# Optimization experiments

Hardware: AMD Instinct MI355X
Metric: run time of the kernel (lower is better)

Reference implementation:

```python
import jax, jax.numpy as jnp
import numpy as np

NUM_FEATURES = 1024
NUM_TRAINING = 32768
NUM_EPOCHS = 2
STEP_SIZE = 0.01


def setup_inputs() -> dict:
    key = jax.random.key(0)
    k1, k2, k3 = jax.random.split(key, 3)
    data = jax.random.normal(k1, (NUM_TRAINING, NUM_FEATURES), dtype=jnp.float32)
    label = jax.random.uniform(k2, (NUM_TRAINING,), dtype=jnp.float32)
    theta = jax.random.normal(k3, (NUM_FEATURES,), dtype=jnp.float32)
    return {"data": data, "label": label, "theta": theta}


def reference(data, label, theta):
    data_2d = data.reshape(NUM_TRAINING, NUM_FEATURES)

    def sample_step(theta, xs):
        x, y = xs  # x: [F], y: scalar
        prob = jax.nn.sigmoid(jnp.dot(theta, x))
        theta = theta - STEP_SIZE * (prob - y) * x
        return theta, None

    def epoch_step(theta, _):
        theta, _ = jax.lax.scan(sample_step, theta, (data_2d, label))
        return theta, None

    theta, _ = jax.lax.scan(epoch_step, theta, None, length=NUM_EPOCHS)
    return theta
```

## Files before the change

### kernel.cpp

```cpp
#include <hip/hip_runtime.h>
#include <hip/hip_cooperative_groups.h>

namespace cg = cooperative_groups;

#define F 1024
#define NTRAIN 32768
#define EPOCHS 2
#define STEP 0.01f
#define BB 512
#define NBLK (NTRAIN / BB)
#define PHASES (EPOCHS * NBLK)
#define COOP_WGS 32

#define NL2E 1.4426950408889634f
#define C1K  0.014426950408889634f
#define NLN2 0.69314718055994531f

__device__ __forceinline__ float rdlane(float v, int lane) {
    return __uint_as_float(__builtin_amdgcn_readlane(__float_as_uint(v), (unsigned)lane));
}

__global__ __launch_bounds__(256) void gram_kernel(const float* __restrict__ X,
                                                   float* __restrict__ G,
                                                   float* __restrict__ C,
                                                   int tiles_per_b)
{
    const int wg  = blockIdx.x;
    const int b   = wg / tiles_per_b;
    int rem = wg % tiles_per_b;

    int ti, tj;
    bool isC = (rem >= 36);
    if (!isC) {
        int tij = rem; ti = 0;
        while (tij >= 8 - ti) { tij -= 8 - ti; ++ti; }
        tj = ti + tij;
    } else {
        rem -= 36; ti = rem >> 3; tj = rem & 7;
    }

    __shared__ __align__(16) float At[16][68];
    __shared__ __align__(16) float Bt[16][68];

    const int t  = threadIdx.x;
    const int tx = t & 15, ty = t >> 4;
    const int sr = t >> 2, sc = (t & 3) * 4;

    const int rowBlk = isC ? ((b + 1) & (NBLK - 1)) : b;
    const float* Xa = X + (size_t)(rowBlk * BB + ti * 64) * F;
    const float* Xb = X + (size_t)(b * BB + tj * 64) * F;
    float* Ob = (isC ? C : G) + (size_t)b * BB * BB;

    float acc[4][4];
#pragma unroll
    for (int p = 0; p < 4; ++p)
#pragma unroll
        for (int q = 0; q < 4; ++q) acc[p][q] = 0.f;

    for (int kc = 0; kc < F; kc += 16) {
        float4 va = *(const float4*)(Xa + (size_t)sr * F + kc + sc);
        float4 vb = *(const float4*)(Xb + (size_t)sr * F + kc + sc);
        __syncthreads();
        At[sc + 0][sr] = va.x; At[sc + 1][sr] = va.y; At[sc + 2][sr] = va.z; At[sc + 3][sr] = va.w;
        Bt[sc + 0][sr] = vb.x; Bt[sc + 1][sr] = vb.y; Bt[sc + 2][sr] = vb.z; Bt[sc + 3][sr] = vb.w;
        __syncthreads();
#pragma unroll
        for (int k = 0; k < 16; ++k) {
            float4 a4 = *(const float4*)&At[k][ty * 4];
            float4 b4 = *(const float4*)&Bt[k][tx * 4];
            acc[0][0] = fmaf(a4.x, b4.x, acc[0][0]);
            acc[0][1] = fmaf(a4.x, b4.y, acc[0][1]);
            acc[0][2] = fmaf(a4.x, b4.z, acc[0][2]);
            acc[0][3] = fmaf(a4.x, b4.w, acc[0][3]);
            acc[1][0] = fmaf(a4.y, b4.x, acc[1][0]);
            acc[1][1] = fmaf(a4.y, b4.y, acc[1][1]);
            acc[1][2] = fmaf(a4.y, b4.z, acc[1][2]);
            acc[1][3] = fmaf(a4.y, b4.w, acc[1][3]);
            acc[2][0] = fmaf(a4.z, b4.x, acc[2][0]);
            acc[2][1] = fmaf(a4.z, b4.y, acc[2][1]);
            acc[2][2] = fmaf(a4.z, b4.z, acc[2][2]);
            acc[2][3] = fmaf(a4.z, b4.w, acc[2][3]);
            acc[3][0] = fmaf(a4.w, b4.x, acc[3][0]);
            acc[3][1] = fmaf(a4.w, b4.y, acc[3][1]);
            acc[3][2] = fmaf(a4.w, b4.z, acc[3][2]);
            acc[3][3] = fmaf(a4.w, b4.w, acc[3][3]);
        }
    }

#pragma unroll
    for (int p = 0; p < 4; ++p) {
        int i = ti * 64 + ty * 4 + p;
        float4 v = make_float4(acc[p][0], acc[p][1], acc[p][2], acc[p][3]);
        *(float4*)(Ob + (size_t)i * BB + tj * 64 + tx * 4) = v;
    }
    if (!isC && ti != tj) {
#pragma unroll
        for (int p = 0; p < 4; ++p)
#pragma unroll
            for (int q = 0; q < 4; ++q)
                Ob[(size_t)(tj * 64 + tx * 4 + q) * BB + ti * 64 + ty * 4 + p] = acc[p][q];
    }
}

__global__ __launch_bounds__(256) void sgd_coop2(
    const float* __restrict__ X, const float* __restrict__ label,
    const float* __restrict__ theta0, float* __restrict__ out,
    const float* __restrict__ G, const float* __restrict__ C,
    float* __restrict__ theta, float* __restrict__ sbuf,
    float* __restrict__ spre, float* __restrict__ wbuf)
{
    cg::grid_group grid = cg::this_grid();
    const int tid = threadIdx.x;
    const int wg  = blockIdx.x;

    if (wg < 4) theta[wg * 256 + tid] = theta0[wg * 256 + tid];
    grid.sync();

    {
        const int wv = (wg << 2) | (tid >> 6);
        const int L  = tid & 63;
        const float4* th4 = (const float4*)theta;
        float4 t4[4];
#pragma unroll
        for (int m = 0; m < 4; ++m) t4[m] = th4[L + 64 * m];
        for (int rr = 0; rr < 4; ++rr) {
            const int r = wv * 4 + rr;
            const float4* xr = (const float4*)(X + (size_t)r * F);
            float acc = 0.f;
#pragma unroll
            for (int m = 0; m < 4; ++m) {
                float4 x4 = xr[L + 64 * m];
                acc = fmaf(x4.x, t4[m].x, acc);
                acc = fmaf(x4.y, t4[m].y, acc);
                acc = fmaf(x4.z, t4[m].z, acc);
                acc = fmaf(x4.w, t4[m].w, acc);
            }
#pragma unroll
            for (int off = 32; off > 0; off >>= 1)
                acc += __shfl_xor(acc, off, 64);
            if (L == 0) sbuf[r] = acc;
        }
    }
    grid.sync();

    for (int p = 0; p < PHASES; ++p) {
        const int blk = p & (NBLK - 1);

        if (wg == 0) {
            if (tid < 64) {
                const int L = tid;
                const float* Gb = G + (size_t)blk * BB * BB;
                const float4* s4 = (const float4*)sbuf;
                float4 z04 = s4[L * 2], z14 = s4[L * 2 + 1];
                float zac[8] = {-NL2E * z04.x, -NL2E * z04.y, -NL2E * z04.z, -NL2E * z04.w,
                                -NL2E * z14.x, -NL2E * z14.y, -NL2E * z14.z, -NL2E * z14.w};
                const float4* y4 = (const float4*)(label + blk * BB);
                float4 ya = y4[L * 2], yb = y4[L * 2 + 1];
                float c2[8] = {-C1K * ya.x, -C1K * ya.y, -C1K * ya.z, -C1K * ya.w,
                               -C1K * yb.x, -C1K * yb.y, -C1K * yb.z, -C1K * yb.w};

                float4 gb0[8], gb1[8];
#pragma unroll
                for (int u = 0; u < 8; ++u) {
                    const float4* gr = (const float4*)(Gb + (size_t)u * BB) + L * 2;
                    gb0[u] = gr[0]; gb1[u] = gr[1];
                }

                for (int i8 = 0; i8 < 64; ++i8) {
                    float wout[8];
#pragma unroll
                    for (int u = 0; u < 8; ++u) {
                        float zs = rdlane(zac[u], i8);
                        float cc = rdlane(c2[u], i8);
                        float E    = __builtin_amdgcn_exp2f(zs);
                        float prob = __builtin_amdgcn_rcpf(1.0f + E);
                        float wv2  = fmaf(C1K, prob, cc);
                        wout[u] = wv2 * -NLN2;
                        float ga[8] = {gb0[u].x, gb0[u].y, gb0[u].z, gb0[u].w,
                                       gb1[u].x, gb1[u].y, gb1[u].z, gb1[u].w};
#pragma unroll
                        for (int jj = 0; jj < 8; ++jj) {
                            int j = (u + 1 + jj) & 7;
                            zac[j] = fmaf(wv2, ga[j], zac[j]);
                        }
                        if (i8 < 63) {
                            const float4* gr =
                                (const float4*)(Gb + (size_t)((i8 + 1) * 8 + u) * BB) + L * 2;
                            gb0[u] = gr[0]; gb1[u] = gr[1];
                        }
                    }
                    if (L == i8) {
                        float4* wp = (float4*)(wbuf + i8 * 8);
                        wp[0] = make_float4(wout[0], wout[1], wout[2], wout[3]);
                        wp[1] = make_float4(wout[4], wout[5], wout[6], wout[7]);
                    }
                }
            }
        } else if (p + 1 < PHASES) {
            const int w = (wg - 1) * 4 + (tid >> 6);
            const int L = tid & 63;
            const int nblk = (p + 1) & (NBLK - 1);
            const float4* th4 = (const float4*)theta;
            float4 t4[4];
#pragma unroll
            for (int m = 0; m < 4; ++m) t4[m] = th4[L + 64 * m];
            for (int r = w; r < BB; r += 124) {
                const float4* xr = (const float4*)(X + (size_t)(nblk * BB + r) * F);
                float acc = 0.f;
#pragma unroll
                for (int m = 0; m < 4; ++m) {
                    float4 x4 = xr[L + 64 * m];
                    acc = fmaf(x4.x, t4[m].x, acc);
                    acc = fmaf(x4.y, t4[m].y, acc);
                    acc = fmaf(x4.z, t4[m].z, acc);
                    acc = fmaf(x4.w, t4[m].w, acc);
                }
#pragma unroll
                for (int off = 32; off > 0; off >>= 1)
                    acc += __shfl_xor(acc, off, 64);
                if (L == 0) spre[r] = acc;
            }
        }
        grid.sync();

        if (wg < 16) {
            __shared__ float red[4][64];
            const int j  = wg * 64 + (tid & 63);
            const int rg = tid >> 6;
            const float* Xb = X + (size_t)blk * BB * F;
            float acc = 0.f;
            for (int ii = 0; ii < 128; ++ii) {
                const int i = rg * 128 + ii;
                acc = fmaf(wbuf[i], Xb[(size_t)i * F + j], acc);
            }
            red[rg][tid & 63] = acc;
            __syncthreads();
            if (tid < 64) {
                float v = theta[j] + red[0][tid] + red[1][tid] + red[2][tid] + red[3][tid];
                theta[j] = v;
                if (p == PHASES - 1) out[j] = v;
            }
        } else if (p + 1 < PHASES) {
            const int w2 = (wg - 16) * 4 + (tid >> 6);
            const int L  = tid & 63;
            const float* Cb = C + (size_t)blk * BB * BB;
            const float4* w4 = (const float4*)wbuf;
            float4 wa = w4[L * 2], wb4 = w4[L * 2 + 1];
            for (int rr = 0; rr < 8; ++rr) {
                const int r = w2 * 8 + rr;
                const float4* cr = (const float4*)(Cb + (size_t)r * BB) + L * 2;
                float4 c0 = cr[0], c1r = cr[1];
                float acc = c0.x * wa.x;
                acc = fmaf(c0.y, wa.y, acc);
                acc = fmaf(c0.z, wa.z, acc);
                acc = fmaf(c0.w, wa.w, acc);
                acc = fmaf(c1r.x, wb4.x, acc);
                acc = fmaf(c1r.y, wb4.y, acc);
                acc = fmaf(c1r.z, wb4.z, acc);
                acc = fmaf(c1r.w, wb4.w, acc);
#pragma unroll
                for (int off = 32; off > 0; off >>= 1)
                    acc += __shfl_xor(acc, off, 64);
                if (L == 0) sbuf[r] = spre[r] + acc;
            }
        }
        grid.sync();
    }
}

__global__ __launch_bounds__(256) void sgd_coop(
    const float* __restrict__ X, const float* __restrict__ label,
    const float* __restrict__ theta0, float* __restrict__ out,
    const float* __restrict__ G, float* __restrict__ theta,
    float* __restrict__ sbuf, float* __restrict__ wbuf)
{
    cg::grid_group grid = cg::this_grid();
    const int tid = threadIdx.x;
    const int wg  = blockIdx.x;

    if (wg < 4) theta[wg * 256 + tid] = theta0[wg * 256 + tid];
    grid.sync();

    auto sgemv = [&](int blk) {
        const int wv = (wg << 2) | (tid >> 6);
        const int L  = tid & 63;
        const float4* th4 = (const float4*)theta;
        float4 t4[4];
#pragma unroll
        for (int m = 0; m < 4; ++m) t4[m] = th4[L + 64 * m];
        for (int rr = 0; rr < 4; ++rr) {
            const int r = wv * 4 + rr;
            const float4* xr = (const float4*)(X + (size_t)(blk * BB + r) * F);
            float acc = 0.f;
#pragma unroll
            for (int m = 0; m < 4; ++m) {
                float4 x4 = xr[L + 64 * m];
                acc = fmaf(x4.x, t4[m].x, acc);
                acc = fmaf(x4.y, t4[m].y, acc);
                acc = fmaf(x4.z, t4[m].z, acc);
                acc = fmaf(x4.w, t4[m].w, acc);
            }
#pragma unroll
            for (int off = 32; off > 0; off >>= 1)
                acc += __shfl_xor(acc, off, 64);
            if (L == 0) sbuf[r] = acc;
        }
    };

    sgemv(0);
    grid.sync();

    for (int p = 0; p < PHASES; ++p) {
        const int blk = p & (NBLK - 1);
        if (wg == 0 && tid < 64) {
            const int L = tid;
            const float* Gb = G + (size_t)blk * BB * BB;
            const float4* s4 = (const float4*)sbuf;
            float4 z04 = s4[L * 2], z14 = s4[L * 2 + 1];
            float zac[8] = {z04.x, z04.y, z04.z, z04.w, z14.x, z14.y, z14.z, z14.w};
            const float4* y4 = (const float4*)(label + blk * BB);
            float4 ya = y4[L * 2], yb = y4[L * 2 + 1];
            float yv[8] = {ya.x, ya.y, ya.z, ya.w, yb.x, yb.y, yb.z, yb.w};
            float4 gb0[8], gb1[8];
#pragma unroll
            for (int u = 0; u < 8; ++u) {
                const float4* gr = (const float4*)(Gb + (size_t)u * BB) + L * 2;
                gb0[u] = gr[0]; gb1[u] = gr[1];
            }
            for (int i8 = 0; i8 < 64; ++i8) {
                float wout[8];
#pragma unroll
                for (int u = 0; u < 8; ++u) {
                    float zi = rdlane(zac[u], i8);
                    float yi = rdlane(yv[u], i8);
                    float E    = __builtin_amdgcn_exp2f(zi * -NL2E);
                    float prob = __builtin_amdgcn_rcpf(1.0f + E);
                    float wv   = STEP * (yi - prob);
                    wout[u] = wv;
                    float4 g0 = gb0[u], g1 = gb1[u];
                    zac[0] = fmaf(wv, g0.x, zac[0]);
                    zac[1] = fmaf(wv, g0.y, zac[1]);
                    zac[2] = fmaf(wv, g0.z, zac[2]);
                    zac[3] = fmaf(wv, g0.w, zac[3]);
                    zac[4] = fmaf(wv, g1.x, zac[4]);
                    zac[5] = fmaf(wv, g1.y, zac[5]);
                    zac[6] = fmaf(wv, g1.z, zac[6]);
                    zac[7] = fmaf(wv, g1.w, zac[7]);
                    if (i8 < 63) {
                        const float4* gr =
                            (const float4*)(Gb + (size_t)((i8 + 1) * 8 + u) * BB) + L * 2;
                        gb0[u] = gr[0]; gb1[u] = gr[1];
                    }
                }
                if (L == i8) {
                    float4* wp = (float4*)(wbuf + i8 * 8);
                    wp[0] = make_float4(wout[0], wout[1], wout[2], wout[3]);
                    wp[1] = make_float4(wout[4], wout[5], wout[6], wout[7]);
                }
            }
        }
        grid.sync();

        if (wg < 16) {
            __shared__ float red[4][64];
            const int j  = wg * 64 + (tid & 63);
            const int rg = tid >> 6;
            const float* Xb = X + (size_t)blk * BB * F;
            float acc = 0.f;
            for (int ii = 0; ii < 128; ++ii) {
                const int i = rg * 128 + ii;
                acc = fmaf(wbuf[i], Xb[(size_t)i * F + j], acc);
            }
            red[rg][tid & 63] = acc;
            __syncthreads();
            if (tid < 64) {
                float v = theta[j] + red[0][tid] + red[1][tid] + red[2][tid] + red[3][tid];
                theta[j] = v;
                if (p == PHASES - 1) out[j] = v;
            }
        }
        grid.sync();

        if (p + 1 < PHASES) sgemv((p + 1) & (NBLK - 1));
        grid.sync();
    }
}

__global__ __launch_bounds__(64, 1) void sgd_seq_kernel(
    const float* __restrict__ data, const float* __restrict__ label,
    const float* __restrict__ theta_in, float* __restrict__ theta_out)
{
    const int lane = threadIdx.x;
    const float4* data4  = (const float4*)data;
    const float4* th4_in = (const float4*)theta_in;
    float4 th[4];
#pragma unroll
    for (int j = 0; j < 4; ++j) th[j] = th4_in[j * 64 + lane];
    float4 xv[4], xn[4];
#pragma unroll
    for (int j = 0; j < 4; ++j) xv[j] = data4[j * 64 + lane];
    float y = label[0];
    const int total = EPOCHS * NTRAIN;
    for (int it = 0; it < total; ++it) {
        int nn = it + 1;
        int nidx = (nn >= total) ? 0 : (nn & (NTRAIN - 1));
        const float4* xp = data4 + (size_t)nidx * (F / 4);
#pragma unroll
        for (int j = 0; j < 4; ++j) xn[j] = xp[j * 64 + lane];
        float ynext = label[nidx];
        float p0 = xv[0].x * th[0].x; p0 = fmaf(xv[0].y, th[0].y, p0);
        p0 = fmaf(xv[0].z, th[0].z, p0); p0 = fmaf(xv[0].w, th[0].w, p0);
        float p1 = xv[1].x * th[1].x; p1 = fmaf(xv[1].y, th[1].y, p1);
        p1 = fmaf(xv[1].z, th[1].z, p1); p1 = fmaf(xv[1].w, th[1].w, p1);
        float p2 = xv[2].x * th[2].x; p2 = fmaf(xv[2].y, th[2].y, p2);
        p2 = fmaf(xv[2].z, th[2].z, p2); p2 = fmaf(xv[2].w, th[2].w, p2);
        float p3 = xv[3].x * th[3].x; p3 = fmaf(xv[3].y, th[3].y, p3);
        p3 = fmaf(xv[3].z, th[3].z, p3); p3 = fmaf(xv[3].w, th[3].w, p3);
        float p = (p0 + p1) + (p2 + p3);
#pragma unroll
        for (int off = 32; off > 0; off >>= 1) p += __shfl_xor(p, off, 64);
        float e = __builtin_amdgcn_exp2f(-p * NL2E);
        float prob = __builtin_amdgcn_rcpf(1.0f + e);
        float c = STEP * (prob - y);
#pragma unroll
        for (int j = 0; j < 4; ++j) {
            th[j].x = fmaf(-c, xv[j].x, th[j].x);
            th[j].y = fmaf(-c, xv[j].y, th[j].y);
            th[j].z = fmaf(-c, xv[j].z, th[j].z);
            th[j].w = fmaf(-c, xv[j].w, th[j].w);
        }
#pragma unroll
        for (int j = 0; j < 4; ++j) xv[j] = xn[j];
        y = ynext;
    }
    float4* out4 = (float4*)theta_out;
#pragma unroll
    for (int j = 0; j < 4; ++j) out4[j * 64 + lane] = th[j];
}

extern "C" void kernel_launch(void* const* d_in, const int* in_sizes, int n_in,
                              void* d_out, int out_size, void* d_ws, size_t ws_size,
                              hipStream_t stream) {
    (void)in_sizes; (void)n_in; (void)out_size;
    const float* X      = (const float*)d_in[0];
    const float* label  = (const float*)d_in[1];
    const float* theta0 = (const float*)d_in[2];
    float* out = (float*)d_out;

    const size_t gsz   = (size_t)NBLK * BB * BB;
    const size_t need2 = (2 * gsz + F + 3 * BB) * sizeof(float);
    const size_t need1 = (gsz + F + 2 * BB) * sizeof(float);

    if (ws_size >= need2) {
        float* G     = (float*)d_ws;
        float* C     = G + gsz;
        float* theta = C + gsz;
        float* sbuf  = theta + F;
        float* spre  = sbuf + BB;
        float* wbuf  = spre + BB;
        int tiles = 100;
        gram_kernel<<<NBLK * 100, 256, 0, stream>>>(X, G, C, tiles);
        const float* Gc = G; const float* Cc = C;
        void* args[] = {(void*)&X, (void*)&label, (void*)&theta0, (void*)&out,
                        (void*)&Gc, (void*)&Cc, (void*)&theta, (void*)&sbuf,
                        (void*)&spre, (void*)&wbuf};
        hipLaunchCooperativeKernel((void*)sgd_coop2, dim3(COOP_WGS), dim3(256),
                                   args, 0, stream);
    } else if (ws_size >= need1) {
        float* G     = (float*)d_ws;
        float* theta = G + gsz;
        float* sbuf  = theta + F;
        float* wbuf  = sbuf + BB;
        int tiles = 36;
        gram_kernel<<<NBLK * 36, 256, 0, stream>>>(X, G, nullptr, tiles);
        void* args[] = {(void*)&X, (void*)&label, (void*)&theta0, (void*)&out,
                        (void*)&G, (void*)&theta, (void*)&sbuf, (void*)&wbuf};
        hipLaunchCooperativeKernel((void*)sgd_coop, dim3(COOP_WGS), dim3(256),
                                   args, 0, stream);
    } else {
        sgd_seq_kernel<<<1, 64, 0, stream>>>(X, label, theta0, out);
    }
}
```

Measured before the change: 6.713 ms.

## Replace cooperative grid.sync with custom atomic-counter barrier and LDS staging

```diff
diff --git a/kernel.cpp b/kernel.cpp
--- a/kernel.cpp
+++ b/kernel.cpp
@@ -18,6 +18,29 @@
 
 __device__ __forceinline__ float rdlane(float v, int lane) {
     return __uint_as_float(__builtin_amdgcn_readlane(__float_as_uint(v), (unsigned)lane));
+}
+__device__ __forceinline__ float aload(const float* p) {
+    return __hip_atomic_load(p, __ATOMIC_RELAXED, __HIP_MEMORY_SCOPE_AGENT);
+}
+__device__ __forceinline__ void astore(float* p, float v) {
+    __hip_atomic_store(p, v, __ATOMIC_RELAXED, __HIP_MEMORY_SCOPE_AGENT);
+}
+
+__device__ __forceinline__ void gbar(int* cnt, int target, int* budget) {
+    asm volatile("s_waitcnt vmcnt(0) lgkmcnt(0)" ::: "memory");
+    __syncthreads();
+    if (threadIdx.x == 0) {
+        __hip_atomic_fetch_add(cnt, 1, __ATOMIC_RELAXED, __HIP_MEMORY_SCOPE_AGENT);
+        while (__hip_atomic_load(cnt, __ATOMIC_RELAXED, __HIP_MEMORY_SCOPE_AGENT) < target) {
+            __builtin_amdgcn_s_sleep(1);
+            if (--(*budget) <= 0) break;
+        }
+    }
+    __syncthreads();
+}
+
+__global__ void init_kernel(int* cnt) {
+    if (threadIdx.x < 64) cnt[threadIdx.x] = 0;
 }
 
 __global__ __launch_bounds__(256) void gram_kernel(const float* __restrict__ X,
@@ -102,24 +125,28 @@
     }
 }
 
-__global__ __launch_bounds__(256) void sgd_coop2(
+__global__ __launch_bounds__(256, 1) void sgd_coop3(
     const float* __restrict__ X, const float* __restrict__ label,
     const float* __restrict__ theta0, float* __restrict__ out,
     const float* __restrict__ G, const float* __restrict__ C,
     float* __restrict__ theta, float* __restrict__ sbuf,
-    float* __restrict__ spre, float* __restrict__ wbuf)
+    float* __restrict__ spre, float* __restrict__ wbuf,
+    int* __restrict__ cnt)
 {
-    cg::grid_group grid = cg::this_grid();
     const int tid = threadIdx.x;
     const int wg  = blockIdx.x;
-
-    if (wg < 4) theta[wg * 256 + tid] = theta0[wg * 256 + tid];
-    grid.sync();
+    int bt = 0;
+    int budget = 1 << 25;
+
+    __shared__ __align__(16) float lds[1024 + 256];
+
+    if (wg < 4) astore(theta + wg * 256 + tid, theta0[wg * 256 + tid]);
+    bt += COOP_WGS; gbar(cnt, bt, &budget);
 
     {
         const int wv = (wg << 2) | (tid >> 6);
         const int L  = tid & 63;
-        const float4* th4 = (const float4*)theta;
+        const float4* th4 = (const float4*)theta0;
         float4 t4[4];
 #pragma unroll
         for (int m = 0; m < 4; ++m) t4[m] = th4[L + 64 * m];
@@ -138,10 +165,10 @@
 #pragma unroll
             for (int off = 32; off > 0; off >>= 1)
                 acc += __shfl_xor(acc, off, 64);
-            if (L == 0) sbuf[r] = acc;
-        }
-    }
-    grid.sync();
+            if (L == 0) astore(sbuf + r, acc);
+        }
+    }
+    bt += COOP_WGS; gbar(cnt, bt, &budget);
 
     for (int p = 0; p < PHASES; ++p) {
         const int blk = p & (NBLK - 1);
@@ -150,23 +177,25 @@
             if (tid < 64) {
                 const int L = tid;
                 const float* Gb = G + (size_t)blk * BB * BB;
-                const float4* s4 = (const float4*)sbuf;
-                float4 z04 = s4[L * 2], z14 = s4[L * 2 + 1];
-                float zac[8] = {-NL2E * z04.x, -NL2E * z04.y, -NL2E * z04.z, -NL2E * z04.w,
-                                -NL2E * z14.x, -NL2E * z14.y, -NL2E * z14.z, -NL2E * z14.w};
-                const float4* y4 = (const float4*)(label + blk * BB);
-                float4 ya = y4[L * 2], yb = y4[L * 2 + 1];
-                float c2[8] = {-C1K * ya.x, -C1K * ya.y, -C1K * ya.z, -C1K * ya.w,
-                               -C1K * yb.x, -C1K * yb.y, -C1K * yb.z, -C1K * yb.w};
-
-                float4 gb0[8], gb1[8];
+                float zac[8], c2[8];
+#pragma unroll
+                for (int u = 0; u < 8; ++u) {
+                    zac[u] = -NL2E * aload(sbuf + L * 8 + u);
+                    c2[u]  = -C1K * label[blk * BB + L * 8 + u];
+                }
+                float4 A0[16], A1[16];
 #pragma unroll
                 for (int u = 0; u < 8; ++u) {
                     const float4* gr = (const float4*)(Gb + (size_t)u * BB) + L * 2;
-                    gb0[u] = gr[0]; gb1[u] = gr[1];
-                }
-
-                for (int i8 = 0; i8 < 64; ++i8) {
+                    A0[2 * u] = gr[0]; A0[2 * u + 1] = gr[1];
+                }
+#pragma unroll
+                for (int u = 0; u < 8; ++u) {
+                    const float4* gr = (const float4*)(Gb + (size_t)(8 + u) * BB) + L * 2;
+                    A1[2 * u] = gr[0]; A1[2 * u + 1] = gr[1];
+                }
+
+                auto step8 = [&](int i8, float4* P) {
                     float wout[8];
 #pragma unroll
                     for (int u = 0; u < 8; ++u) {
@@ -176,34 +205,44 @@
                         float prob = __builtin_amdgcn_rcpf(1.0f + E);
                         float wv2  = fmaf(C1K, prob, cc);
                         wout[u] = wv2 * -NLN2;
-                        float ga[8] = {gb0[u].x, gb0[u].y, gb0[u].z, gb0[u].w,
-                                       gb1[u].x, gb1[u].y, gb1[u].z, gb1[u].w};
+                        float4 g0 = P[2 * u], g1 = P[2 * u + 1];
+                        int nr = (i8 + 2) * 8 + u;
+                        if (nr < BB) {
+                            const float4* gr =
+                                (const float4*)(Gb + (size_t)nr * BB) + L * 2;
+                            P[2 * u] = gr[0]; P[2 * u + 1] = gr[1];
+                        }
+                        float ga[8] = {g0.x, g0.y, g0.z, g0.w,
+                                       g1.x, g1.y, g1.z, g1.w};
 #pragma unroll
                         for (int jj = 0; jj < 8; ++jj) {
                             int j = (u + 1 + jj) & 7;
                             zac[j] = fmaf(wv2, ga[j], zac[j]);
                         }
-                        if (i8 < 63) {
-                            const float4* gr =
-                                (const float4*)(Gb + (size_t)((i8 + 1) * 8 + u) * BB) + L * 2;
-                            gb0[u] = gr[0]; gb1[u] = gr[1];
-                        }
                     }
                     if (L == i8) {
-                        float4* wp = (float4*)(wbuf + i8 * 8);
-                        wp[0] = make_float4(wout[0], wout[1], wout[2], wout[3]);
-                        wp[1] = make_float4(wout[4], wout[5], wout[6], wout[7]);
+#pragma unroll
+                        for (int u = 0; u < 8; ++u)
+                            astore(wbuf + i8 * 8 + u, wout[u]);
                     }
+                };
+
+                for (int i8 = 0; i8 < 64; i8 += 2) {
+                    step8(i8, A0);
+                    step8(i8 + 1, A1);
                 }
             }
         } else if (p + 1 < PHASES) {
+#pragma unroll
+            for (int m = 0; m < 4; ++m)
+                lds[tid + 256 * m] = aload(theta + tid + 256 * m);
+            __syncthreads();
             const int w = (wg - 1) * 4 + (tid >> 6);
             const int L = tid & 63;
             const int nblk = (p + 1) & (NBLK - 1);
-            const float4* th4 = (const float4*)theta;
             float4 t4[4];
 #pragma unroll
-            for (int m = 0; m < 4; ++m) t4[m] = th4[L + 64 * m];
+            for (int m = 0; m < 4; ++m) t4[m] = ((const float4*)lds)[L + 64 * m];
             for (int r = w; r < BB; r += 124) {
                 const float4* xr = (const float4*)(X + (size_t)(nblk * BB + r) * F);
                 float acc = 0.f;
@@ -218,34 +257,41 @@
 #pragma unroll
                 for (int off = 32; off > 0; off >>= 1)
                     acc += __shfl_xor(acc, off, 64);
-                if (L == 0) spre[r] = acc;
-            }
-        }
-        grid.sync();
+                if (L == 0) astore(spre + r, acc);
+            }
+        }
+        bt += COOP_WGS; gbar(cnt, bt, &budget);
 
         if (wg < 16) {
-            __shared__ float red[4][64];
+            lds[tid] = aload(wbuf + tid);
+            lds[tid + 256] = aload(wbuf + tid + 256);
+            __syncthreads();
             const int j  = wg * 64 + (tid & 63);
             const int rg = tid >> 6;
             const float* Xb = X + (size_t)blk * BB * F;
             float acc = 0.f;
             for (int ii = 0; ii < 128; ++ii) {
                 const int i = rg * 128 + ii;
-                acc = fmaf(wbuf[i], Xb[(size_t)i * F + j], acc);
-            }
-            red[rg][tid & 63] = acc;
+                acc = fmaf(lds[i], Xb[(size_t)i * F + j], acc);
+            }
+            __syncthreads();
+            lds[1024 + rg * 64 + (tid & 63)] = acc;
             __syncthreads();
             if (tid < 64) {
-                float v = theta[j] + red[0][tid] + red[1][tid] + red[2][tid] + red[3][tid];
-                theta[j] = v;
+                float v = aload(theta + j) + lds[1024 + tid] + lds[1024 + 64 + tid] +
+                          lds[1024 + 128 + tid] + lds[1024 + 192 + tid];
+                astore(theta + j, v);
                 if (p == PHASES - 1) out[j] = v;
             }
         } else if (p + 1 < PHASES) {
+            lds[tid] = aload(wbuf + tid);
+            lds[tid + 256] = aload(wbuf + tid + 256);
+            __syncthreads();
             const int w2 = (wg - 16) * 4 + (tid >> 6);
             const int L  = tid & 63;
             const float* Cb = C + (size_t)blk * BB * BB;
-            const float4* w4 = (const float4*)wbuf;
-            float4 wa = w4[L * 2], wb4 = w4[L * 2 + 1];
+            float4 wa = ((const float4*)lds)[L * 2];
+            float4 wb4 = ((const float4*)lds)[L * 2 + 1];
             for (int rr = 0; rr < 8; ++rr) {
                 const int r = w2 * 8 + rr;
                 const float4* cr = (const float4*)(Cb + (size_t)r * BB) + L * 2;
@@ -261,10 +307,10 @@
 #pragma unroll
                 for (int off = 32; off > 0; off >>= 1)
                     acc += __shfl_xor(acc, off, 64);
-                if (L == 0) sbuf[r] = spre[r] + acc;
-            }
-        }
-        grid.sync();
+                if (L == 0) astore(sbuf + r, aload(spre + r) + acc);
+            }
+        }
+        bt += COOP_WGS; gbar(cnt, bt, &budget);
     }
 }
 
@@ -448,7 +494,7 @@
     float* out = (float*)d_out;
 
     const size_t gsz   = (size_t)NBLK * BB * BB;
-    const size_t need2 = (2 * gsz + F + 3 * BB) * sizeof(float);
+    const size_t need2 = (2 * gsz + F + 3 * BB + 64) * sizeof(float);
     const size_t need1 = (gsz + F + 2 * BB) * sizeof(float);
 
     if (ws_size >= need2) {
@@ -458,21 +504,17 @@
         float* sbuf  = theta + F;
         float* spre  = sbuf + BB;
         float* wbuf  = spre + BB;
-        int tiles = 100;
-        gram_kernel<<<NBLK * 100, 256, 0, stream>>>(X, G, C, tiles);
-        const float* Gc = G; const float* Cc = C;
-        void* args[] = {(void*)&X, (void*)&label, (void*)&theta0, (void*)&out,
-                        (void*)&Gc, (void*)&Cc, (void*)&theta, (void*)&sbuf,
-                        (void*)&spre, (void*)&wbuf};
-        hipLaunchCooperativeKernel((void*)sgd_coop2, dim3(COOP_WGS), dim3(256),
-                                   args, 0, stream);
+        int*   cnt   = (int*)(wbuf + BB);
+        init_kernel<<<1, 64, 0, stream>>>(cnt);
+        gram_kernel<<<NBLK * 100, 256, 0, stream>>>(X, G, C, 100);
+        sgd_coop3<<<COOP_WGS, 256, 0, stream>>>(X, label, theta0, out,
+                                                G, C, theta, sbuf, spre, wbuf, cnt);
     } else if (ws_size >= need1) {
         float* G     = (float*)d_ws;
         float* theta = G + gsz;
         float* sbuf  = theta + F;
         float* wbuf  = sbuf + BB;
-        int tiles = 36;
-        gram_kernel<<<NBLK * 36, 256, 0, stream>>>(X, G, nullptr, tiles);
+        gram_kernel<<<NBLK * 36, 256, 0, stream>>>(X, G, nullptr, 36);
         void* args[] = {(void*)&X, (void*)&label, (void*)&theta0, (void*)&out,
                         (void*)&G, (void*)&theta, (void*)&sbuf, (void*)&wbuf};
         hipLaunchCooperativeKernel((void*)sgd_coop, dim3(COOP_WGS), dim3(256),
```

New measurement: 9.848 ms. 46.7% more time.
